# Kernel tuning notes

Hardware: AMD Instinct MI355X
Metric: run time of the kernel (lower is better)

## Reference

```python
import jax, jax.numpy as jnp
import numpy as np

NUM_FIELDS = 50
CARD = 10000  # per-field cardinality; global index = x + field_offset
FACTOR_DIM = 64
ATT_SIZE = 64
BATCH = 2048


def setup_inputs() -> dict:
    key = jax.random.key(0)
    ks = jax.random.split(key, 5)
    x = jax.random.randint(ks[0], (BATCH, NUM_FIELDS), 0, CARD, dtype=jnp.int64)
    emb = jax.random.normal(ks[1], (NUM_FIELDS * CARD, FACTOR_DIM), jnp.float32) * 0.1
    W1 = jax.random.normal(ks[2], (FACTOR_DIM, ATT_SIZE), jnp.float32) * 0.1
    b1 = jnp.zeros((ATT_SIZE,), jnp.float32)
    w2 = jax.random.normal(ks[3], (ATT_SIZE, 1), jnp.float32) * 0.1
    b2 = jnp.zeros((1,), jnp.float32)
    lin_w = jax.random.normal(ks[4], (NUM_FIELDS * CARD, 1), jnp.float32) * 0.1
    lin_b = jnp.zeros((1,), jnp.float32)
    return {"x": x, "emb": emb, "W1": W1, "b1": b1, "w2": w2, "b2": b2,
            "lin_w": lin_w, "lin_b": lin_b}


def reference(x, emb, W1, b1, w2, b2, lin_w, lin_b):
    F = NUM_FIELDS
    offsets = (jnp.arange(F, dtype=x.dtype) * CARD)[None, :]  # [1, F]
    idx = x + offsets                                          # [B, F] global ids
    factors = emb[idx]                                         # [B, F, D]
    iu, ju = np.triu_indices(F, k=1)                           # P = F*(F-1)/2 pairs (i < j)
    inter = factors[:, iu, :] * factors[:, ju, :]              # [B, P, D]
    # attention MLP: Dense -> ReLU -> Dense(1) -> Softmax over pair axis
    h = jax.nn.relu(jnp.einsum('bpd,da->bpa', inter, W1) + b1)
    logits = jnp.einsum('bpa,ao->bpo', h, w2) + b2             # [B, P, 1]
    scores = jax.nn.softmax(logits, axis=1)
    inter_sum = jnp.sum(inter, axis=-1, keepdims=True)         # [B, P, 1]
    attended = jnp.sum(inter_sum * scores, axis=1)             # [B, 1]
    linear = jnp.sum(lin_w[idx], axis=1) + lin_b               # [B, 1]
    return linear + attended
```

## Files before the change

kernel.cpp:

```cpp
#include <hip/hip_runtime.h>
#include <hip/hip_bf16.h>

#define NF 50
#define NCARD 10000
#define FD 64
#define NPAIR 1225
#define NPAIR_PAD 1232
#define NTILE 77
#define NB 2
#define FROWB 144
#define FBATB 7200

typedef _Float16 h16x8 __attribute__((ext_vector_type(8)));
typedef float f32x4 __attribute__((ext_vector_type(4)));

__global__ void afm_pre(const float* __restrict__ W1,
                        _Float16* __restrict__ w1f,
                        unsigned* __restrict__ poffg) {
    const int bid = blockIdx.x, tid = threadIdx.x;
    if (bid < 2) {
        const int slot = bid * 4 + (tid >> 6);
        const int lane = tid & 63;
        const int n16 = lane & 15, quad = lane >> 4;
        const int mt = slot >> 1, ks = slot & 1;
        const int a = mt * 16 + n16;
        h16x8 v;
        #pragma unroll
        for (int jj = 0; jj < 8; ++jj) {
            int k = ks * 32 + quad * 8 + jj;
            v[jj] = (_Float16)W1[k * 64 + a];
        }
        *(h16x8*)(w1f + ((size_t)(slot * 64 + lane)) * 8) = v;
    } else {
        int p = (bid - 2) * 256 + tid;
        if (p < NPAIR_PAD) {
            int i = 0, j = 0;
            if (p < NPAIR) {
                float disc = (float)((2 * NF - 1) * (2 * NF - 1) - 8 * p);
                i = (int)(((float)(2 * NF - 1) - sqrtf(disc)) * 0.5f);
                if (i < 0) i = 0;
                if (i > NF - 2) i = NF - 2;
                while (i + 1 <= NF - 2 && (i + 1) * (NF - 1) - ((i + 1) * i) / 2 <= p) ++i;
                while (i > 0 && i * (NF - 1) - (i * (i - 1)) / 2 > p) --i;
                j = p - (i * (NF - 1) - (i * (i - 1)) / 2) + i + 1;
            }
            poffg[p] = (unsigned)(i * FROWB) | ((unsigned)(j * FROWB) << 16);
        }
    }
}

__global__ __launch_bounds__(256) void afm_main(
    const int* __restrict__ x,
    const float* __restrict__ emb,
    const float* __restrict__ b1,
    const float* __restrict__ w2,
    const float* __restrict__ lin_w,
    const float* __restrict__ lin_b,
    const _Float16* __restrict__ w1f,
    const unsigned* __restrict__ poffg,
    float* __restrict__ out)
{
    __shared__ __align__(16) _Float16 fach[NB * 50 * 72];
    __shared__ float cmb[4][3];

    const int b0   = blockIdx.x * NB;
    const int tid  = threadIdx.x;
    const int lane = tid & 63;
    const int wid  = tid >> 6;
    const int n16  = lane & 15;
    const int quad = lane >> 4;

    for (int t = tid; t < NB * 50 * 8; t += 256) {
        int rowid = t >> 3, q = t & 7;
        int bb = (rowid >= 50) ? 1 : 0;
        int f = rowid - bb * 50;
        int gid = x[(b0 + bb) * NF + f] + f * NCARD;
        const float* src = emb + (size_t)gid * FD + q * 8;
        float4 v0 = *(const float4*)(src);
        float4 v1 = *(const float4*)(src + 4);
        h16x8 h;
        h[0] = (_Float16)v0.x; h[1] = (_Float16)v0.y;
        h[2] = (_Float16)v0.z; h[3] = (_Float16)v0.w;
        h[4] = (_Float16)v1.x; h[5] = (_Float16)v1.y;
        h[6] = (_Float16)v1.z; h[7] = (_Float16)v1.w;
        *(h16x8*)(fach + bb * 3600 + f * 72 + q * 8) = h;
    }

    h16x8 afragW[8];
    #pragma unroll
    for (int s = 0; s < 8; ++s)
        afragW[s] = *(const h16x8*)(w1f + ((size_t)(s * 64 + lane)) * 8);
    h16x8 aones;
    {
        _Float16 o = (n16 == 0) ? (_Float16)1.0f : (_Float16)0.0f;
        #pragma unroll
        for (int jj = 0; jj < 8; ++jj) aones[jj] = o;
    }
    f32x4 b1v[4], w2v[4];
    #pragma unroll
    for (int mt = 0; mt < 4; ++mt) {
        const float4 bb = *(const float4*)(b1 + mt * 16 + quad * 4);
        const float4 ww = *(const float4*)(w2 + mt * 16 + quad * 4);
        b1v[mt] = (f32x4){bb.x, bb.y, bb.z, bb.w};
        w2v[mt] = (f32x4){ww.x, ww.y, ww.z, ww.w};
    }
    __syncthreads();

    const int mybatch = wid >> 1;
    const char* fb = (const char*)fach + mybatch * FBATB;
    float m = -1e30f, se = 0.f, sei = 0.f;

    for (int t = (wid & 1); t < NTILE; t += 2) {
        const unsigned po = poffg[t * 16 + n16];
        const char* pbi = fb + (po & 0xFFFFu) + quad * 16;
        const char* pbj = fb + (po >> 16) + quad * 16;

        h16x8 pr0 = (*(const h16x8*)(pbi)) * (*(const h16x8*)(pbj));
        h16x8 pr1 = (*(const h16x8*)(pbi + 64)) * (*(const h16x8*)(pbj + 64));

        f32x4 accS = __builtin_amdgcn_mfma_f32_16x16x32_f16(aones, pr0, (f32x4){0.f, 0.f, 0.f, 0.f}, 0, 0, 0);
        accS = __builtin_amdgcn_mfma_f32_16x16x32_f16(aones, pr1, accS, 0, 0, 0);

        float lacc = 0.f;
        #pragma unroll
        for (int mt = 0; mt < 4; ++mt) {
            f32x4 acc = __builtin_amdgcn_mfma_f32_16x16x32_f16(afragW[mt * 2 + 0], pr0, b1v[mt], 0, 0, 0);
            acc = __builtin_amdgcn_mfma_f32_16x16x32_f16(afragW[mt * 2 + 1], pr1, acc, 0, 0, 0);
            #pragma unroll
            for (int r = 0; r < 4; ++r)
                lacc += fmaxf(acc[r], 0.f) * w2v[mt][r];
        }
        lacc += __shfl_xor(lacc, 16, 64);
        lacc += __shfl_xor(lacc, 32, 64);
        float is = __shfl(accS[0], n16, 64);

        if (t * 16 + n16 >= NPAIR) lacc = -1e30f;

        float nm = fmaxf(m, lacc);
        float sc = __expf(m - nm);
        float e  = __expf(lacc - nm);
        se  = se * sc + e;
        sei = sei * sc + e * is;
        m = nm;
    }

    #pragma unroll
    for (int d = 1; d <= 8; d <<= 1) {
        float m2   = __shfl_xor(m, d, 64);
        float se2  = __shfl_xor(se, d, 64);
        float sei2 = __shfl_xor(sei, d, 64);
        float nm = fmaxf(m, m2);
        float a = __expf(m - nm), bsc = __expf(m2 - nm);
        se  = se * a + se2 * bsc;
        sei = sei * a + sei2 * bsc;
        m = nm;
    }

    float lin = 0.f;
    if ((wid & 1) == 0) {
        if (lane < NF) {
            int gid = x[(b0 + mybatch) * NF + lane] + lane * NCARD;
            lin = lin_w[gid];
        }
        #pragma unroll
        for (int d = 1; d <= 32; d <<= 1) lin += __shfl_xor(lin, d, 64);
    }

    if (lane == 0) { cmb[wid][0] = m; cmb[wid][1] = se; cmb[wid][2] = sei; }
    __syncthreads();
    if ((wid & 1) == 0 && lane == 0) {
        float m2 = cmb[wid + 1][0], se2 = cmb[wid + 1][1], sei2 = cmb[wid + 1][2];
        float nm = fmaxf(m, m2);
        float a = __expf(m - nm), bsc = __expf(m2 - nm);
        float tse  = se * a + se2 * bsc;
        float tsei = sei * a + sei2 * bsc;
        out[b0 + mybatch] = lin + lin_b[0] + tsei / tse;
    }
}

extern "C" void kernel_launch(void* const* d_in, const int* in_sizes, int n_in,
                              void* d_out, int out_size, void* d_ws, size_t ws_size,
                              hipStream_t stream) {
    const int*   x     = (const int*)d_in[0];
    const float* emb   = (const float*)d_in[1];
    const float* W1    = (const float*)d_in[2];
    const float* b1    = (const float*)d_in[3];
    const float* w2    = (const float*)d_in[4];
    const float* lin_w = (const float*)d_in[6];
    const float* lin_b = (const float*)d_in[7];
    float* out = (float*)d_out;

    _Float16* w1f   = (_Float16*)d_ws;
    unsigned* poffg = (unsigned*)((char*)d_ws + 8192);

    afm_pre<<<7, 256, 0, stream>>>(W1, w1f, poffg);
    const int batch = out_size;
    afm_main<<<batch / NB, 256, 0, stream>>>(x, emb, b1, w2, lin_w, lin_b, w1f, poffg, out);
}
```

Before: 220.4 us.

## Replace pair lookup table with 4x4 field-group tiling and drop pre-kernel

Fields are padded to 52 and pairs are walked as 4x4 blocks of field groups (gi<=gj), so each lane reuses its row-i fragments across the inner loop. Invalid pairs (i>=j or j>=50) are masked in the online softmax. This removes the precomputed pair-offset table, its per-tile global load and the shuffle for the interaction sum. The W1 fragment-building pre-kernel is also removed: every block now converts W1 to fp16 fragments itself from global memory. A (256,4) launch bound is added. The trade-off is roughly 91 tiles per batch instead of 77, because diagonal and padded tiles are partly wasted, plus redundant per-block W1 gather loads.

```diff
diff --git a/kernel.cpp b/kernel.cpp
--- a/kernel.cpp
+++ b/kernel.cpp
@@ -2,65 +2,28 @@
 #include <hip/hip_bf16.h>
 
 #define NF 50
+#define NFP 52
+#define NG 13
 #define NCARD 10000
 #define FD 64
-#define NPAIR 1225
-#define NPAIR_PAD 1232
-#define NTILE 77
 #define NB 2
-#define FROWB 144
-#define FBATB 7200
+#define FROW 72
+#define FBAT (NFP * FROW)
 
 typedef _Float16 h16x8 __attribute__((ext_vector_type(8)));
 typedef float f32x4 __attribute__((ext_vector_type(4)));
 
-__global__ void afm_pre(const float* __restrict__ W1,
-                        _Float16* __restrict__ w1f,
-                        unsigned* __restrict__ poffg) {
-    const int bid = blockIdx.x, tid = threadIdx.x;
-    if (bid < 2) {
-        const int slot = bid * 4 + (tid >> 6);
-        const int lane = tid & 63;
-        const int n16 = lane & 15, quad = lane >> 4;
-        const int mt = slot >> 1, ks = slot & 1;
-        const int a = mt * 16 + n16;
-        h16x8 v;
-        #pragma unroll
-        for (int jj = 0; jj < 8; ++jj) {
-            int k = ks * 32 + quad * 8 + jj;
-            v[jj] = (_Float16)W1[k * 64 + a];
-        }
-        *(h16x8*)(w1f + ((size_t)(slot * 64 + lane)) * 8) = v;
-    } else {
-        int p = (bid - 2) * 256 + tid;
-        if (p < NPAIR_PAD) {
-            int i = 0, j = 0;
-            if (p < NPAIR) {
-                float disc = (float)((2 * NF - 1) * (2 * NF - 1) - 8 * p);
-                i = (int)(((float)(2 * NF - 1) - sqrtf(disc)) * 0.5f);
-                if (i < 0) i = 0;
-                if (i > NF - 2) i = NF - 2;
-                while (i + 1 <= NF - 2 && (i + 1) * (NF - 1) - ((i + 1) * i) / 2 <= p) ++i;
-                while (i > 0 && i * (NF - 1) - (i * (i - 1)) / 2 > p) --i;
-                j = p - (i * (NF - 1) - (i * (i - 1)) / 2) + i + 1;
-            }
-            poffg[p] = (unsigned)(i * FROWB) | ((unsigned)(j * FROWB) << 16);
-        }
-    }
-}
-
-__global__ __launch_bounds__(256) void afm_main(
+__global__ __launch_bounds__(256, 4) void afm_main(
     const int* __restrict__ x,
     const float* __restrict__ emb,
+    const float* __restrict__ W1,
     const float* __restrict__ b1,
     const float* __restrict__ w2,
     const float* __restrict__ lin_w,
     const float* __restrict__ lin_b,
-    const _Float16* __restrict__ w1f,
-    const unsigned* __restrict__ poffg,
     float* __restrict__ out)
 {
-    __shared__ __align__(16) _Float16 fach[NB * 50 * 72];
+    __shared__ __align__(16) _Float16 fach[NB * FBAT];
     __shared__ float cmb[4][3];
 
     const int b0   = blockIdx.x * NB;
@@ -70,32 +33,38 @@
     const int n16  = lane & 15;
     const int quad = lane >> 4;
 
-    for (int t = tid; t < NB * 50 * 8; t += 256) {
+    for (int t = tid; t < NB * NFP * 8; t += 256) {
         int rowid = t >> 3, q = t & 7;
-        int bb = (rowid >= 50) ? 1 : 0;
-        int f = rowid - bb * 50;
-        int gid = x[(b0 + bb) * NF + f] + f * NCARD;
-        const float* src = emb + (size_t)gid * FD + q * 8;
-        float4 v0 = *(const float4*)(src);
-        float4 v1 = *(const float4*)(src + 4);
-        h16x8 h;
-        h[0] = (_Float16)v0.x; h[1] = (_Float16)v0.y;
-        h[2] = (_Float16)v0.z; h[3] = (_Float16)v0.w;
-        h[4] = (_Float16)v1.x; h[5] = (_Float16)v1.y;
-        h[6] = (_Float16)v1.z; h[7] = (_Float16)v1.w;
-        *(h16x8*)(fach + bb * 3600 + f * 72 + q * 8) = h;
+        int bb = (rowid >= NFP) ? 1 : 0;
+        int f = rowid - bb * NFP;
+        h16x8 h = {0, 0, 0, 0, 0, 0, 0, 0};
+        if (f < NF) {
+            int gid = x[(b0 + bb) * NF + f] + f * NCARD;
+            const float* src = emb + (size_t)gid * FD + q * 8;
+            float4 v0 = *(const float4*)(src);
+            float4 v1 = *(const float4*)(src + 4);
+            h[0] = (_Float16)v0.x; h[1] = (_Float16)v0.y;
+            h[2] = (_Float16)v0.z; h[3] = (_Float16)v0.w;
+            h[4] = (_Float16)v1.x; h[5] = (_Float16)v1.y;
+            h[6] = (_Float16)v1.z; h[7] = (_Float16)v1.w;
+        }
+        *(h16x8*)(fach + (size_t)rowid * FROW + q * 8) = h;
     }
 
     h16x8 afragW[8];
     #pragma unroll
-    for (int s = 0; s < 8; ++s)
-        afragW[s] = *(const h16x8*)(w1f + ((size_t)(s * 64 + lane)) * 8);
-    h16x8 aones;
-    {
-        _Float16 o = (n16 == 0) ? (_Float16)1.0f : (_Float16)0.0f;
+    for (int mt = 0; mt < 4; ++mt) {
         #pragma unroll
-        for (int jj = 0; jj < 8; ++jj) aones[jj] = o;
+        for (int ks = 0; ks < 2; ++ks) {
+            h16x8 v;
+            #pragma unroll
+            for (int jj = 0; jj < 8; ++jj)
+                v[jj] = (_Float16)W1[(ks * 32 + quad * 8 + jj) * 64 + mt * 16 + n16];
+            afragW[mt * 2 + ks] = v;
+        }
     }
+    h16x8 aones = {(_Float16)1, (_Float16)1, (_Float16)1, (_Float16)1,
+                   (_Float16)1, (_Float16)1, (_Float16)1, (_Float16)1};
     f32x4 b1v[4], w2v[4];
     #pragma unroll
     for (int mt = 0; mt < 4; ++mt) {
@@ -107,41 +76,47 @@
     __syncthreads();
 
     const int mybatch = wid >> 1;
-    const char* fb = (const char*)fach + mybatch * FBATB;
+    const _Float16* fb = fach + mybatch * FBAT;
+    const int a4 = n16 >> 2, b4 = n16 & 3;
+    const int gi_lo = (wid & 1) ? 4 : 0;
+    const int gi_hi = (wid & 1) ? NG : 4;
+
     float m = -1e30f, se = 0.f, sei = 0.f;
 
-    for (int t = (wid & 1); t < NTILE; t += 2) {
-        const unsigned po = poffg[t * 16 + n16];
-        const char* pbi = fb + (po & 0xFFFFu) + quad * 16;
-        const char* pbj = fb + (po >> 16) + quad * 16;
+    for (int gi = gi_lo; gi < gi_hi; ++gi) {
+        const int i = gi * 4 + a4;
+        const _Float16* ri = fb + (size_t)i * FROW + quad * 8;
+        const h16x8 ri0 = *(const h16x8*)(ri);
+        const h16x8 ri1 = *(const h16x8*)(ri + 32);
+        for (int gj = gi; gj < NG; ++gj) {
+            const int j = gj * 4 + b4;
+            const _Float16* rj = fb + (size_t)j * FROW + quad * 8;
+            h16x8 pr0 = ri0 * (*(const h16x8*)(rj));
+            h16x8 pr1 = ri1 * (*(const h16x8*)(rj + 32));
 
-        h16x8 pr0 = (*(const h16x8*)(pbi)) * (*(const h16x8*)(pbj));
-        h16x8 pr1 = (*(const h16x8*)(pbi + 64)) * (*(const h16x8*)(pbj + 64));
+            f32x4 accS = __builtin_amdgcn_mfma_f32_16x16x32_f16(aones, pr0, (f32x4){0.f, 0.f, 0.f, 0.f}, 0, 0, 0);
+            accS = __builtin_amdgcn_mfma_f32_16x16x32_f16(aones, pr1, accS, 0, 0, 0);
 
-        f32x4 accS = __builtin_amdgcn_mfma_f32_16x16x32_f16(aones, pr0, (f32x4){0.f, 0.f, 0.f, 0.f}, 0, 0, 0);
-        accS = __builtin_amdgcn_mfma_f32_16x16x32_f16(aones, pr1, accS, 0, 0, 0);
+            float lacc = 0.f;
+            #pragma unroll
+            for (int mt = 0; mt < 4; ++mt) {
+                f32x4 acc = __builtin_amdgcn_mfma_f32_16x16x32_f16(afragW[mt * 2 + 0], pr0, b1v[mt], 0, 0, 0);
+                acc = __builtin_amdgcn_mfma_f32_16x16x32_f16(afragW[mt * 2 + 1], pr1, acc, 0, 0, 0);
+                #pragma unroll
+                for (int r = 0; r < 4; ++r)
+                    lacc += fmaxf(acc[r], 0.f) * w2v[mt][r];
+            }
+            lacc += __shfl_xor(lacc, 16, 64);
+            lacc += __shfl_xor(lacc, 32, 64);
 
-        float lacc = 0.f;
-        #pragma unroll
-        for (int mt = 0; mt < 4; ++mt) {
-            f32x4 acc = __builtin_amdgcn_mfma_f32_16x16x32_f16(afragW[mt * 2 + 0], pr0, b1v[mt], 0, 0, 0);
-            acc = __builtin_amdgcn_mfma_f32_16x16x32_f16(afragW[mt * 2 + 1], pr1, acc, 0, 0, 0);
-            #pragma unroll
-            for (int r = 0; r < 4; ++r)
-                lacc += fmaxf(acc[r], 0.f) * w2v[mt][r];
+            const bool valid = (i < j) && (j < NF);
+            float nm = fmaxf(m, valid ? lacc : -1e30f);
+            float sc = __expf(m - nm);
+            float e  = valid ? __expf(lacc - nm) : 0.f;
+            se  = se * sc + e;
+            sei = sei * sc + e * accS[0];
+            m = nm;
         }
-        lacc += __shfl_xor(lacc, 16, 64);
-        lacc += __shfl_xor(lacc, 32, 64);
-        float is = __shfl(accS[0], n16, 64);
-
-        if (t * 16 + n16 >= NPAIR) lacc = -1e30f;
-
-        float nm = fmaxf(m, lacc);
-        float sc = __expf(m - nm);
-        float e  = __expf(lacc - nm);
-        se  = se * sc + e;
-        sei = sei * sc + e * is;
-        m = nm;
     }
 
     #pragma unroll
@@ -189,11 +164,6 @@
     const float* lin_w = (const float*)d_in[6];
     const float* lin_b = (const float*)d_in[7];
     float* out = (float*)d_out;
-
-    _Float16* w1f   = (_Float16*)d_ws;
-    unsigned* poffg = (unsigned*)((char*)d_ws + 8192);
-
-    afm_pre<<<7, 256, 0, stream>>>(W1, w1f, poffg);
     const int batch = out_size;
-    afm_main<<<batch / NB, 256, 0, stream>>>(x, emb, b1, w2, lin_w, lin_b, w1f, poffg, out);
+    afm_main<<<batch / NB, 256, 0, stream>>>(x, emb, W1, b1, w2, lin_w, lin_b, out);
 }
```

Result: no change. 217.2 us (-1.5%).
